# Kernel tuning notes

Hardware: AMD Instinct MI355X
Metric: run time of the kernel (lower is better)

Reference implementation:

```python
import jax, jax.numpy as jnp
import numpy as np

NEG_INF = -jnp.inf


def setup_inputs() -> dict:
    key = jax.random.key(0)
    k1, k2, k3, k4 = jax.random.split(key, 4)
    B, V = 256, 128000
    logits = jax.random.normal(k1, (B, V), dtype=jnp.float32)
    temperatures = jax.random.uniform(k2, (B,), dtype=jnp.float32, minval=0.5, maxval=1.5)
    top_ks = jax.random.randint(k3, (B,), 0, 1024, dtype=jnp.int32)
    top_ps = jax.random.uniform(k4, (B,), dtype=jnp.float32)
    return {"logits": logits, "temperatures": temperatures, "top_ks": top_ks, "top_ps": top_ps}


def _filtered_logits(logits, temperatures, top_ks, top_ps):
    # Faithful vectorized version of the per-row torch loops.
    B, V = logits.shape
    x = logits.astype(jnp.float32) / temperatures[:, None]

    # Sort each row descending once; reuse for top-k and top-p.
    order = jnp.argsort(-x, axis=-1)                       # [B, V] desc indices
    sorted_x = jnp.take_along_axis(x, order, axis=-1)      # [B, V]
    ranks = jnp.arange(V)[None, :]                         # [1, V]

    # top-k: active only when 0 < k < V (matches torch branch)
    k = top_ks[:, None].astype(jnp.int32)
    topk_active = (k > 0) & (k < V)
    keep_k = jnp.where(topk_active, ranks < k, True)
    sorted_x = jnp.where(keep_k, sorted_x, NEG_INF)

    # top-p on softmax of top-k-filtered logits. Softmax is order-preserving,
    # so sorted probs == softmax of sorted (filtered) logits.
    sorted_probs = jax.nn.softmax(sorted_x, axis=-1)
    cumsum = jnp.cumsum(sorted_probs, axis=-1)
    p = top_ps[:, None]
    cutoff = jnp.sum(cumsum <= p, axis=-1, keepdims=True)  # (cumsum<=p).sum()
    cutoff = jnp.where(cutoff < V, cutoff + 1, cutoff)     # include next token
    topp_active = (p > 0.0) & (p < 1.0)
    keep_p = jnp.where(topp_active, ranks < cutoff, True)
    sorted_x = jnp.where(keep_p, sorted_x, NEG_INF)

    # Unsort back to original token order.
    inv = jnp.argsort(order, axis=-1)
    return jnp.take_along_axis(sorted_x, inv, axis=-1)


def reference(logits, temperatures, top_ks, top_ps):
    x = _filtered_logits(logits, temperatures, top_ks, top_ps)
    probs = jax.nn.softmax(x, axis=-1)
    # Gumbel-max style sampling: argmax(probs / Exp(1)) (torch .exponential_ trick)
    e = jax.random.exponential(jax.random.key(42), probs.shape, dtype=jnp.float32)
    e = jnp.maximum(e, 1e-10)
    return jnp.argmax(probs / e, axis=-1)
```

## Files before the change

### kernel.cpp

```cpp
#include <hip/hip_runtime.h>
#include <stdint.h>

#define VV 128000
#define BLOCK 1024
#define NB 4096
#define CAP 4096

typedef unsigned long long ull;

__device__ __forceinline__ uint32_t rotl32(uint32_t x, int r){ return (x << r) | (x >> (32 - r)); }

__device__ __forceinline__ float exp_noise(uint32_t f){
  const uint32_t ks0 = 0u, ks1 = 42u, ks2 = 0x1BD11BDAu ^ 0u ^ 42u;
  uint32_t x0 = 0u + ks0;
  uint32_t x1 = f + ks1;
#define R1(r) { x0 += x1; x1 = rotl32(x1, r); x1 ^= x0; }
  R1(13) R1(15) R1(26) R1(6)   x0 += ks1; x1 += ks2 + 1u;
  R1(17) R1(29) R1(16) R1(24)  x0 += ks2; x1 += ks0 + 2u;
  R1(13) R1(15) R1(26) R1(6)   x0 += ks0; x1 += ks1 + 3u;
  R1(17) R1(29) R1(16) R1(24)  x0 += ks1; x1 += ks2 + 4u;
  R1(13) R1(15) R1(26) R1(6)   x0 += ks2; x1 += ks0 + 5u;
#undef R1
  uint32_t bits = x0 ^ x1;
  float u = __uint_as_float((bits >> 9) | 0x3F800000u) - 1.0f;
  float e = -log1pf(-u);
  return fmaxf(e, 1e-10f);
}

__device__ __forceinline__ uint32_t fkey(float x){
  uint32_t u = __float_as_uint(x);
  return u ^ ((u & 0x80000000u) ? 0xFFFFFFFFu : 0x80000000u);
}
__device__ __forceinline__ float keyval(uint32_t k){
  uint32_t bits = (k & 0x80000000u) ? (k ^ 0x80000000u) : ~k;
  return __uint_as_float(bits);
}

__device__ void suffix_scan_u(uint32_t* h, uint32_t* tmp, int tid){
  const int base = tid * 4;
  uint32_t l0=h[base], l1=h[base+1], l2=h[base+2], l3=h[base+3];
  uint32_t s3=l3, s2=l2+s3, s1=l1+s2, s0=l0+s1;
  tmp[tid] = s0; __syncthreads();
  for (int d=1; d<BLOCK; d<<=1){
    uint32_t add = (tid+d<BLOCK) ? tmp[tid+d] : 0u;
    __syncthreads();
    tmp[tid] += add;
    __syncthreads();
  }
  uint32_t E = (tid+1<BLOCK) ? tmp[tid+1] : 0u;
  h[base]=s0+E; h[base+1]=s1+E; h[base+2]=s2+E; h[base+3]=s3+E;
  __syncthreads();
}
__device__ void suffix_scan_f(float* h, float* tmp, int tid){
  const int base = tid * 4;
  float l0=h[base], l1=h[base+1], l2=h[base+2], l3=h[base+3];
  float s3=l3, s2=l2+s3, s1=l1+s2, s0=l0+s1;
  tmp[tid] = s0; __syncthreads();
  for (int d=1; d<BLOCK; d<<=1){
    float add = (tid+d<BLOCK) ? tmp[tid+d] : 0.f;
    __syncthreads();
    tmp[tid] += add;
    __syncthreads();
  }
  float E = (tid+1<BLOCK) ? tmp[tid+1] : 0.f;
  h[base]=s0+E; h[base+1]=s1+E; h[base+2]=s2+E; h[base+3]=s3+E;
  __syncthreads();
}

__device__ uint32_t select_tth_smallest(uint32_t* a, int n, int t){
  for (int i=0;i<t;i++){
    int mi=i; uint32_t mv=a[i];
    for (int j=i+1;j<n;j++) if (a[j]<mv){ mv=a[j]; mi=j; }
    a[mi]=a[i]; a[i]=mv;
  }
  return a[t-1];
}

__device__ void bitonic_sort(ull* a, int N, int tid){
  for (int len=2; len<=N; len<<=1){
    for (int j=len>>1; j>0; j>>=1){
      for (int i=tid; i<N; i+=BLOCK){
        int l = i ^ j;
        if (l > i){
          ull x = a[i], y = a[l];
          bool asc = ((i & len) == 0);
          if (asc ? (x > y) : (x < y)){ a[i]=y; a[l]=x; }
        }
      }
      __syncthreads();
    }
  }
}

#define ROW4R_BEGIN \
    for (int c0 = tid; c0 < VV/4; c0 += BLOCK*4){ \
      float4 qv[4]; int cb[4]; bool gv[4]; \
      _Pragma("unroll") \
      for (int t=0;t<4;t++){ int cc = c0 + t*BLOCK; gv[t] = (cc < VV/4); cb[t] = cc*4; if (gv[t]) qv[t] = rp[cc]; } \
      _Pragma("unroll") \
      for (int t=0;t<4;t++) if (gv[t]){ \
        float vs[4] = {qv[t].x, qv[t].y, qv[t].z, qv[t].w}; \
        _Pragma("unroll") \
        for (int j=0;j<4;j++){ \
          uint32_t u = fkey(vs[j]); \
          uint32_t idx = (uint32_t)(cb[t]+j); \
          (void)idx;
#define ROW4R_END } } }

#define ROW4_BEGIN \
    for (int c0 = tid; c0 < VV/4; c0 += BLOCK*4){ \
      float4 qv[4]; int cb[4]; bool gv[4]; \
      _Pragma("unroll") \
      for (int t=0;t<4;t++){ int cc = c0 + t*BLOCK; gv[t] = (cc < VV/4); cb[t] = cc*4; if (gv[t]) qv[t] = rp[cc]; } \
      _Pragma("unroll") \
      for (int t=0;t<4;t++) if (gv[t]){ \
        float xs[4] = {qv[t].x, qv[t].y, qv[t].z, qv[t].w}; \
        _Pragma("unroll") \
        for (int j=0;j<4;j++){ \
          float x = xs[j]/T; \
          uint32_t u = fkey(x); \
          uint32_t idx = (uint32_t)(cb[t]+j); \
          (void)idx;
#define ROW4_END } } }

__global__ __launch_bounds__(BLOCK) void sampler_kernel(
    const float* __restrict__ logits, const float* __restrict__ temps,
    const int* __restrict__ topks, const float* __restrict__ topps,
    int* __restrict__ out)
{
  __shared__ __align__(16) uint8_t SM[102400];
  uint32_t* h4    = (uint32_t*)SM;
  ull*      cand  = (ull*)SM;
  uint32_t* h2    = (uint32_t*)(SM + 32*1024);
  ull*      sort2 = (ull*)(SM + 48*1024);
  float*    S     = (float*)SM;
  float*    wf    = (float*)(SM + 16*1024);
  uint32_t* wu    = (uint32_t*)(SM + 64*1024);
  float*    tmpf  = (float*)(SM + 80*1024);
  uint32_t* tmpu  = (uint32_t*)(SM + 84*1024);
  float*    ck    = (float*)(SM + 88*1024);
  ull*      red   = (ull*)(SM + 92*1024);

  __shared__ int s_idx, s_n, s_n2, s_tk, s_ntk, s_tp, s_ntp;
  __shared__ uint32_t s_uk, s_idxk, s_up, s_idxp;
  __shared__ float s_m, s_Zk, s_Ztot;

  const int b   = blockIdx.x;
  const int tid = threadIdx.x;
  const float T = temps[b];
  const int   k = topks[b];
  const float p = topps[b];
  const float* row = logits + (size_t)b * VV;
  const float4* rp = reinterpret_cast<const float4*>(row);
  const bool topk_act = (k > 0) && (k < VV);
  const bool topp_act = (p > 0.0f) && (p < 1.0f);

  if (topk_act){
    for (int i=tid;i<4*NB;i+=BLOCK) h4[i]=0u;
    __syncthreads();
    ROW4R_BEGIN
      atomicAdd(&h4[((u>>20)<<2) | (uint32_t)(tid&3)], 1u);
    ROW4R_END
    __syncthreads();
    for (int i=tid;i<NB;i+=BLOCK)
      wu[i] = h4[(i<<2)] + h4[(i<<2)|1] + h4[(i<<2)|2] + h4[(i<<2)|3];
    __syncthreads();
    suffix_scan_u(wu, tmpu, tid);
    if (tid==0) s_idx = 0;
    __syncthreads();
    for (int i=tid;i<NB;i+=BLOCK){
      uint32_t a  = wu[i];
      uint32_t nn = (i+1<NB) ? wu[i+1] : 0u;
      if (a >= (uint32_t)k && nn < (uint32_t)k) s_idx = i;
    }
    __syncthreads();
    const uint32_t beta = (uint32_t)s_idx;
    const int n = (int)wu[beta];
    const uint32_t c_above = (beta+1<NB) ? wu[beta+1] : 0u;
    if (n <= CAP){
      if (tid==0) s_n = 0;
      __syncthreads();
      ROW4R_BEGIN
        if ((u>>20) >= beta){
          int pos = atomicAdd(&s_n, 1);
          cand[pos] = (((ull)(~u))<<32) | idx;
        }
      ROW4R_END
      __syncthreads();
      ull* srt; int m;
      if (n <= 1024){ srt = cand; m = n; }
      else {
        for (int i=tid;i<NB;i+=BLOCK) h2[i]=0u;
        __syncthreads();
        for (int i=tid;i<n;i+=BLOCK){
          uint32_t u2 = ~(uint32_t)(cand[i]>>32);
          if ((u2>>20) == beta) atomicAdd(&h2[(u2>>8)&0xFFFu], 1u);
        }
        __syncthreads();
        suffix_scan_u(h2, tmpu, tid);
        const uint32_t kr = (uint32_t)k - c_above;
        if (tid==0) s_idx = 0;
        __syncthreads();
        for (int i=tid;i<NB;i+=BLOCK){
          uint32_t a  = h2[i];
          uint32_t nn = (i+1<NB) ? h2[i+1] : 0u;
          if (a >= kr && nn < kr) s_idx = i;
        }
        __syncthreads();
        const uint32_t gam = (uint32_t)s_idx;
        const int np = (int)(c_above + h2[gam]);
        if (np <= 1024){
          if (tid==0) s_n2 = 0;
          __syncthreads();
          const uint32_t cut24 = (beta<<12) | gam;
          for (int i=tid;i<n;i+=BLOCK){
            ull e = cand[i];
            uint32_t u2 = ~(uint32_t)(e>>32);
            if ((u2>>8) >= cut24){
              int pos = atomicAdd(&s_n2, 1);
              sort2[pos] = e;
            }
          }
          __syncthreads();
          srt = sort2; m = np;
        } else { srt = cand; m = n; }
      }
      int N = 2; while (N < m) N <<= 1;
      for (int i=tid;i<N;i+=BLOCK) if (i >= m) srt[i] = 0xFFFFFFFFFFFFFFFFull;
      __syncthreads();
      bitonic_sort(srt, N, tid);
      const int kk = k;
      const float xm = keyval(~(uint32_t)(srt[0]>>32)) / T;
      float w = 0.f; uint32_t myidx = 0u;
      if (tid < kk){
        ull e = srt[tid];
        myidx = (uint32_t)e;
        float xv = keyval(~(uint32_t)(e>>32)) / T;
        w = expf(xv - xm);
      }
      ck[tid] = w; __syncthreads();
      for (int d=BLOCK/2; d>0; d>>=1){
        if (tid < d) ck[tid] += ck[tid+d];
        __syncthreads();
      }
      if (tid==0) s_Ztot = ck[0];
      __syncthreads();
      const float Zk = s_Ztot;
      ck[tid] = w / Zk; __syncthreads();
      for (int d=1; d<BLOCK; d<<=1){
        float add = (tid >= d) ? ck[tid-d] : 0.f;
        __syncthreads();
        ck[tid] += add;
        __syncthreads();
      }
      tmpu[tid] = (tid < kk && ck[tid] <= p) ? 1u : 0u;
      __syncthreads();
      for (int d=BLOCK/2; d>0; d>>=1){
        if (tid < d) tmpu[tid] += tmpu[tid+d];
        __syncthreads();
      }
      int L;
      if (!topp_act) L = kk;
      else { int c = (int)tmpu[0]; L = (c >= kk) ? kk : (c + 1); }
      ull best = 0ull;
      if (tid < L){
        float q = w / exp_noise((uint32_t)b * (uint32_t)VV + myidx);
        best = (((ull)__float_as_uint(q)) << 32) | (uint32_t)(~myidx);
      }
      red[tid] = best; __syncthreads();
      for (int d=BLOCK/2; d>0; d>>=1){
        if (tid < d){ ull o = red[tid+d]; if (o > red[tid]) red[tid] = o; }
        __syncthreads();
      }
      if (tid==0) out[b] = (int)(~(uint32_t)(red[0] & 0xFFFFFFFFull));
      return;
    }
    __syncthreads();
  }

  for (int i=tid;i<NB;i+=BLOCK){ S[i]=0.f; wu[i]=0u; }
  __syncthreads();
  float lmax = -3.4e38f;
  ROW4_BEGIN
    lmax = fmaxf(lmax, x);
    atomicAdd(&wu[u>>20], 1u);
    atomicAdd(&S[u>>20], expf(x));
  ROW4_END
  tmpf[tid] = lmax; __syncthreads();
  for (int d=BLOCK/2; d>0; d>>=1){
    if (tid < d) tmpf[tid] = fmaxf(tmpf[tid], tmpf[tid+d]);
    __syncthreads();
  }
  if (tid==0) s_m = tmpf[0];
  __syncthreads();
  suffix_scan_u(wu, tmpu, tid);
  suffix_scan_f(S,  tmpf, tid);

  uint32_t uk = 0u, idxk = 0xFFFFFFFFu;
  int bk1 = -1;
  if (topk_act){
    if (tid==0) s_idx = 0;
    __syncthreads();
    for (int i=tid;i<NB;i+=BLOCK){
      uint32_t a  = wu[i];
      uint32_t nn = (i+1<NB) ? wu[i+1] : 0u;
      if (a >= (uint32_t)k && nn < (uint32_t)k) s_idx = i;
    }
    __syncthreads();
    bk1 = s_idx;
    const uint32_t c_above1 = (bk1+1<NB) ? wu[bk1+1] : 0u;
    const float    M_above1 = (bk1+1<NB) ? S[bk1+1]  : 0.f;
    __syncthreads();
    for (int i=tid;i<NB;i+=BLOCK){ wu[i]=0u; wf[i]=0.f; }
    __syncthreads();
    ROW4_BEGIN
      if ((int)(u>>20) == bk1){
        atomicAdd(&wu[(u>>8)&0xFFFu], 1u);
        atomicAdd(&wf[(u>>8)&0xFFFu], expf(x));
      }
    ROW4_END
    __syncthreads();
    suffix_scan_u(wu, tmpu, tid);
    suffix_scan_f(wf, tmpf, tid);
    if (tid==0) s_idx = 0;
    __syncthreads();
    for (int i=tid;i<NB;i+=BLOCK){
      uint32_t a  = c_above1 + wu[i];
      uint32_t nn = c_above1 + ((i+1<NB) ? wu[i+1] : 0u);
      if (a >= (uint32_t)k && nn < (uint32_t)k) s_idx = i;
    }
    __syncthreads();
    const int bk2 = s_idx;
    const uint32_t c_above2 = c_above1 + ((bk2+1<NB) ? wu[bk2+1] : 0u);
    const float    M_above2 = M_above1 + ((bk2+1<NB) ? wf[bk2+1] : 0.f);
    __syncthreads();
    if (tid < 256){ wu[tid]=0u; wf[tid]=0.f; }
    __syncthreads();
    const uint32_t top24k = (((uint32_t)bk1)<<12) | (uint32_t)bk2;
    ROW4_BEGIN
      if ((u>>8) == top24k){
        atomicAdd(&wu[u & 0xFFu], 1u);
        atomicAdd(&wf[u & 0xFFu], expf(x));
      }
    ROW4_END
    __syncthreads();
    if (tid==0){
      uint32_t r = 0u; float mr = 0.f; int b3 = 0;
      for (int i=255;i>=0;--i){
        if (c_above2 + r + wu[i] >= (uint32_t)k){ b3 = i; break; }
        r += wu[i]; mr += wf[i];
      }
      const uint32_t cgt = c_above2 + r;
      const float mgt = M_above2 + mr;
      const int nt = (int)wu[b3];
      const int tk = k - (int)cgt;
      s_uk  = (((uint32_t)bk1)<<20) | (((uint32_t)bk2)<<8) | (uint32_t)b3;
      s_tk  = tk; s_ntk = nt;
      s_Zk  = mgt + (float)tk * expf(keyval(s_uk));
      s_n   = 0;
    }
    __syncthreads();
    uk = s_uk;
    if (s_tk < s_ntk){
      ROW4_BEGIN
        if (u == uk){
          int pos = atomicAdd(&s_n, 1);
          if (pos < NB) wu[pos] = idx;
        }
      ROW4_END
      __syncthreads();
      if (tid==0){
        int n2 = min(s_n, NB);
        int t  = min(s_tk, n2);
        s_idxk = select_tth_smallest(wu, n2, t);
      }
      __syncthreads();
      idxk = s_idxk;
    }
  }
  const float Zk = topk_act ? s_Zk : S[0];

  uint32_t up = 0u, idxp = 0xFFFFFFFFu;
  const float tgt = p * Zk;
  const bool pall = (!topp_act) || (tgt >= Zk);
  if (!pall){
    if (tid==0) s_idx = -2;
    __syncthreads();
    for (int i=tid;i<NB;i+=BLOCK){
      if (i > bk1){
        float a  = S[i];
        float nn = (i+1<NB) ? S[i+1] : 0.f;
        if (a > tgt && nn <= tgt) s_idx = i;
      }
    }
    __syncthreads();
    int bp1 = (s_idx >= 0) ? s_idx : bk1;
    if (bp1 < 0) bp1 = 0;
    const float Mab = (bp1+1<NB) ? S[bp1+1] : 0.f;
    __syncthreads();
    for (int i=tid;i<NB;i+=BLOCK) wf[i]=0.f;
    __syncthreads();
    ROW4_BEGIN
      if ((int)(u>>20) == bp1){
        bool kk_ok = (!topk_act) || (u > uk) || (u == uk && idx <= idxk);
        if (kk_ok) atomicAdd(&wf[(u>>8)&0xFFFu], expf(x));
      }
    ROW4_END
    __syncthreads();
    suffix_scan_f(wf, tmpf, tid);
    if (tid==0) s_idx = -2;
    __syncthreads();
    for (int i=tid;i<NB;i+=BLOCK){
      float a  = Mab + wf[i];
      float nn = Mab + ((i+1<NB) ? wf[i+1] : 0.f);
      if (a > tgt && nn <= tgt) s_idx = i;
    }
    __syncthreads();
    int bp2;
    if (s_idx >= 0){ bp2 = s_idx; }
    else {
      if (tid==0) s_idx = NB;
      __syncthreads();
      for (int i=tid;i<NB;i+=BLOCK){
        float a  = wf[i];
        float nn = (i+1<NB) ? wf[i+1] : 0.f;
        if (a > nn) atomicMin(&s_idx, i);
      }
      __syncthreads();
      bp2 = (s_idx < NB) ? s_idx : 0;
    }
    const float Mab2 = Mab + ((bp2+1<NB) ? wf[bp2+1] : 0.f);
    __syncthreads();
    if (tid < 256){ wf[tid]=0.f; wu[tid]=0u; }
    __syncthreads();
    const uint32_t top24p = (((uint32_t)bp1)<<12) | (uint32_t)bp2;
    ROW4_BEGIN
      if ((u>>8) == top24p){
        bool kk_ok = (!topk_act) || (u > uk) || (u == uk && idx <= idxk);
        if (kk_ok){
          atomicAdd(&wf[u & 0xFFu], expf(x));
          atomicAdd(&wu[u & 0xFFu], 1u);
        }
      }
    ROW4_END
    __syncthreads();
    if (tid==0){
      float run = 0.f; int b3 = -1; float mgt = 0.f;
      for (int i=255;i>=0;--i){
        float sufn = run; run += wf[i];
        if (Mab2 + run > tgt && Mab2 + sufn <= tgt){ b3 = i; mgt = Mab2 + sufn; break; }
      }
      if (b3 < 0){
        float run2 = 0.f;
        for (int i=255;i>=0;--i){
          if (wu[i] > 0u){ b3 = i; mgt = Mab2 + run2; }
          run2 += wf[i];
        }
        if (b3 < 0){ b3 = 0; mgt = Mab2; }
      }
      const uint32_t upv = (((uint32_t)bp1)<<20) | (((uint32_t)bp2)<<8) | (uint32_t)b3;
      const int ntp = (int)wu[b3];
      const float ev = expf(keyval(upv));
      int t = 0;
      for (int j=1;j<=ntp;j++){
        float before = mgt + (float)(j-1) * ev;
        if (before / Zk <= p) t++; else break;
      }
      if (t < 1) t = 1;
      s_up = upv; s_tp = t; s_ntp = ntp; s_n = 0;
    }
    __syncthreads();
    up = s_up;
    if (s_tp < s_ntp){
      ROW4_BEGIN
        if (u == up){
          bool kk_ok = (!topk_act) || (u > uk) || (u == uk && idx <= idxk);
          if (kk_ok){
            int pos = atomicAdd(&s_n, 1);
            if (pos < NB) wu[pos] = idx;
          }
        }
      ROW4_END
      __syncthreads();
      if (tid==0){
        int n2 = min(s_n, NB);
        int t  = min(s_tp, n2);
        s_idxp = select_tth_smallest(wu, n2, t);
      }
      __syncthreads();
      idxp = s_idxp;
    }
  }

  const float m  = s_m;
  const float Zs = Zk * expf(-m);
  ull best = 0ull;
  ROW4_BEGIN
    bool kk_ok = (!topk_act) || (u > uk) || (u == uk && idx <= idxk);
    bool kp_ok = pall || (u > up) || (u == up && idx <= idxp);
    if (kk_ok && kp_ok){
      float q = (expf(x - m) / Zs) / exp_noise((uint32_t)b * (uint32_t)VV + idx);
      ull pk = (((ull)__float_as_uint(q)) << 32) | (uint32_t)(~idx);
      best = (pk > best) ? pk : best;
    }
  ROW4_END
  red[tid] = best; __syncthreads();
  for (int d=BLOCK/2; d>0; d>>=1){
    if (tid < d){ ull o = red[tid+d]; if (o > red[tid]) red[tid] = o; }
    __syncthreads();
  }
  if (tid==0) out[b] = (int)(~(uint32_t)(red[0] & 0xFFFFFFFFull));
}

extern "C" void kernel_launch(void* const* d_in, const int* in_sizes, int n_in,
                              void* d_out, int out_size, void* d_ws, size_t ws_size,
                              hipStream_t stream) {
  (void)in_sizes; (void)n_in; (void)out_size; (void)d_ws; (void)ws_size;
  const float* logits = (const float*)d_in[0];
  const float* temps  = (const float*)d_in[1];
  const int*   ks     = (const int*)d_in[2];
  const float* ps     = (const float*)d_in[3];
  int* out = (int*)d_out;
  sampler_kernel<<<256, BLOCK, 0, stream>>>(logits, temps, ks, ps, out);
}
```

Before: 231.5 us.

## Split sampler into multi-kernel pipeline with per-row chunked histogram and candidate gather

```diff
diff --git a/kernel.cpp b/kernel.cpp
--- a/kernel.cpp
+++ b/kernel.cpp
@@ -2,9 +2,10 @@
 #include <stdint.h>
 
 #define VV 128000
-#define BLOCK 1024
-#define NB 4096
+#define HN 4096
 #define CAP 4096
+#define CAPR 8192
+#define CHUNK_F4 4000
 
 typedef unsigned long long ull;
 
@@ -36,18 +37,375 @@
   return __uint_as_float(bits);
 }
 
+__device__ uint32_t select_tth_smallest(uint32_t* a, int n, int t){
+  for (int i=0;i<t;i++){
+    int mi=i; uint32_t mv=a[i];
+    for (int j=i+1;j<n;j++) if (a[j]<mv){ mv=a[j]; mi=j; }
+    a[mi]=a[i]; a[i]=mv;
+  }
+  return a[t-1];
+}
+
+template<typename Tv, int NT>
+__device__ __forceinline__ void suffix4096(Tv* h, Tv* parts, int tid){
+  constexpr int E = HN/NT;
+  const int base = tid*E;
+  Tv loc[E]; Tv s = (Tv)0;
+  #pragma unroll
+  for (int i=E-1;i>=0;--i){ s += h[base+i]; loc[i]=s; }
+  const int lane = tid & 63, w = tid >> 6;
+  Tv v = s;
+  #pragma unroll
+  for (int d=1; d<64; d<<=1){
+    Tv o = __shfl_down(v, (unsigned)d, 64);
+    if (lane + d < 64) v += o;
+  }
+  if (lane == 0) parts[w] = v;
+  __syncthreads();
+  Tv woff = (Tv)0;
+  for (int i=w+1;i<NT/64;i++) woff += parts[i];
+  Tv lex = __shfl_down(v, 1u, 64);
+  if (lane == 63) lex = (Tv)0;
+  const Tv off = woff + lex;
+  #pragma unroll
+  for (int i=0;i<E;i++) h[base+i] = loc[i] + off;
+  __syncthreads();
+}
+
+__global__ __launch_bounds__(256) void hist_kernel(const float* __restrict__ logits,
+                                                   uint32_t* __restrict__ hists){
+  __shared__ uint32_t h[HN];
+  const int g = blockIdx.x, r = g >> 3, c = g & 7, tid = threadIdx.x;
+  for (int i=tid;i<HN;i+=256) h[i]=0u;
+  __syncthreads();
+  const float4* rp = reinterpret_cast<const float4*>(logits + (size_t)r*VV) + (size_t)c*CHUNK_F4;
+  for (int c0=tid;c0<CHUNK_F4;c0+=1024){
+    float4 q[4]; bool g4[4];
+    #pragma unroll
+    for (int t=0;t<4;t++){ int cc=c0+t*256; g4[t]=(cc<CHUNK_F4); if(g4[t]) q[t]=rp[cc]; }
+    #pragma unroll
+    for (int t=0;t<4;t++) if(g4[t]){
+      atomicAdd(&h[fkey(q[t].x)>>20],1u);
+      atomicAdd(&h[fkey(q[t].y)>>20],1u);
+      atomicAdd(&h[fkey(q[t].z)>>20],1u);
+      atomicAdd(&h[fkey(q[t].w)>>20],1u);
+    }
+  }
+  __syncthreads();
+  uint32_t* gh = hists + (size_t)r*HN;
+  for (int i=tid;i<HN;i+=256){ uint32_t v=h[i]; if (v) atomicAdd(&gh[i], v); }
+}
+
+__global__ __launch_bounds__(256) void gather_kernel(const float* __restrict__ logits,
+    const int* __restrict__ topks, const uint32_t* __restrict__ hists,
+    uint32_t* __restrict__ ctrs, ull* __restrict__ cands){
+  __shared__ uint32_t h[HN];
+  __shared__ uint32_t parts[4];
+  __shared__ int s_beta;
+  const int g = blockIdx.x, r = g >> 3, c = g & 7, tid = threadIdx.x;
+  const int k = topks[r];
+  if (k < 1 || k >= VV) return;
+  const uint32_t* gh = hists + (size_t)r*HN;
+  for (int i=tid;i<HN;i+=256) h[i] = gh[i];
+  __syncthreads();
+  suffix4096<uint32_t,256>(h, parts, tid);
+  if (tid==0) s_beta = 0;
+  __syncthreads();
+  for (int i=tid;i<HN;i+=256){
+    uint32_t a=h[i], nn=(i+1<HN)?h[i+1]:0u;
+    if (a >= (uint32_t)k && nn < (uint32_t)k) s_beta=i;
+  }
+  __syncthreads();
+  const uint32_t beta=(uint32_t)s_beta;
+  const uint32_t n = h[beta];
+  if (n > CAPR){ if (c==0 && tid==0) ctrs[r] = n; return; }
+  ull* cr = cands + (size_t)r*CAPR;
+  const float4* rp = reinterpret_cast<const float4*>(logits + (size_t)r*VV) + (size_t)c*CHUNK_F4;
+  const uint32_t idx0 = (uint32_t)(c*CHUNK_F4*4);
+  for (int c0=tid;c0<CHUNK_F4;c0+=1024){
+    float4 q[4]; bool g4[4];
+    #pragma unroll
+    for (int t=0;t<4;t++){ int cc=c0+t*256; g4[t]=(cc<CHUNK_F4); if(g4[t]) q[t]=rp[cc]; }
+    #pragma unroll
+    for (int t=0;t<4;t++) if(g4[t]){
+      float vs[4]={q[t].x,q[t].y,q[t].z,q[t].w};
+      #pragma unroll
+      for (int j=0;j<4;j++){
+        uint32_t u=fkey(vs[j]);
+        if ((u>>20) >= beta){
+          uint32_t pos = atomicAdd(&ctrs[r], 1u);
+          cr[pos] = (((ull)u)<<32) | (idx0 + (uint32_t)(c0+t*256)*4u + (uint32_t)j);
+        }
+      }
+    }
+  }
+}
+
+__global__ __launch_bounds__(1024) void select_kernel(
+    const float* __restrict__ temps, const int* __restrict__ topks, const float* __restrict__ topps,
+    const uint32_t* __restrict__ ctrs, const ull* __restrict__ cands, int* __restrict__ outp){
+  __shared__ ull ce[CAPR];
+  __shared__ uint32_t hbu[HN];
+  __shared__ uint32_t c3[256];
+  __shared__ float    f3[256];
+  __shared__ uint32_t tie[2048];
+  __shared__ uint32_t parts_u[16];
+  __shared__ float    parts_f[16];
+  __shared__ ull      parts_m[16];
+  __shared__ int s_i1, s_i2, s_nt, s_tp, s_ntp, s_cnt;
+  __shared__ uint32_t s_um, s_uk, s_idxk, s_up, s_idxp, s_cgt;
+  __shared__ float s_Zk;
+
+  const int r = blockIdx.x, tid = threadIdx.x;
+  const int k = topks[r];
+  if (k < 1 || k >= VV) return;
+  const uint32_t ntot = ctrs[r];
+  if (ntot > CAPR) return;
+  const int n = (int)ntot;
+  const float T = temps[r];
+  const float p = topps[r];
+  const bool topp_act = (p > 0.f) && (p < 1.f);
+  const ull* cr = cands + (size_t)r*CAPR;
+  for (int i=tid;i<n;i+=1024) ce[i] = cr[i];
+  __syncthreads();
+
+  uint32_t um = 0u;
+  for (int i=tid;i<n;i+=1024){ uint32_t u=(uint32_t)(ce[i]>>32); um = um>u?um:u; }
+  {
+    const int lane=tid&63, w=tid>>6; uint32_t v=um;
+    #pragma unroll
+    for (int d=32;d>0;d>>=1){ uint32_t o=__shfl_down(v,(unsigned)d,64); if(lane+d<64 && o>v) v=o; }
+    if (lane==0) parts_u[w]=v;
+    __syncthreads();
+    if (tid==0){ uint32_t m2=0; for(int i=0;i<16;i++) if(parts_u[i]>m2) m2=parts_u[i]; s_um=m2; }
+    __syncthreads();
+    um = s_um;
+  }
+  const float xm = keyval(um)/T;
+
+  for (int i=tid;i<HN;i+=1024) hbu[i]=0u;
+  __syncthreads();
+  for (int i=tid;i<n;i+=1024){ uint32_t u=(uint32_t)(ce[i]>>32); atomicAdd(&hbu[u>>20],1u); }
+  __syncthreads();
+  suffix4096<uint32_t,1024>(hbu, parts_u, tid);
+  if (tid==0) s_i1=0;
+  __syncthreads();
+  for (int i=tid;i<HN;i+=1024){
+    uint32_t a=hbu[i], nn=(i+1<HN)?hbu[i+1]:0u;
+    if (a>=(uint32_t)k && nn<(uint32_t)k) s_i1=i;
+  }
+  __syncthreads();
+  const int b1=s_i1;
+  const uint32_t cA=(b1+1<HN)?hbu[b1+1]:0u;
+  __syncthreads();
+  for (int i=tid;i<HN;i+=1024) hbu[i]=0u;
+  __syncthreads();
+  for (int i=tid;i<n;i+=1024){ uint32_t u=(uint32_t)(ce[i]>>32); if ((int)(u>>20)==b1) atomicAdd(&hbu[(u>>8)&0xFFFu],1u); }
+  __syncthreads();
+  suffix4096<uint32_t,1024>(hbu, parts_u, tid);
+  if (tid==0) s_i2=0;
+  __syncthreads();
+  for (int i=tid;i<HN;i+=1024){
+    uint32_t a=cA+hbu[i], nn=cA+((i+1<HN)?hbu[i+1]:0u);
+    if (a>=(uint32_t)k && nn<(uint32_t)k) s_i2=i;
+  }
+  __syncthreads();
+  const int b2=s_i2;
+  const uint32_t cB=cA+((b2+1<HN)?hbu[b2+1]:0u);
+  if (tid<256) c3[tid]=0u;
+  __syncthreads();
+  const uint32_t t24=((uint32_t)b1<<12)|(uint32_t)b2;
+  for (int i=tid;i<n;i+=1024){ uint32_t u=(uint32_t)(ce[i]>>32); if ((u>>8)==t24) atomicAdd(&c3[u&0xFFu],1u); }
+  __syncthreads();
+  if (tid==0){
+    uint32_t rr=0; int b3=0;
+    for (int i=255;i>=0;--i){ if (cB+rr+c3[i] >= (uint32_t)k){ b3=i; break; } rr+=c3[i]; }
+    s_uk=(t24<<8)|(uint32_t)b3;
+    s_cgt=cB+rr;
+    s_nt=(int)c3[b3];
+    s_cnt=0;
+  }
+  __syncthreads();
+  const uint32_t uk=s_uk;
+  const int tk=k-(int)s_cgt, nt=s_nt;
+  uint32_t idxk=0xFFFFFFFFu;
+  if (tk<nt){
+    for (int i=tid;i<n;i+=1024){
+      ull e=ce[i]; uint32_t u=(uint32_t)(e>>32);
+      if (u==uk){ int pos=atomicAdd(&s_cnt,1); if (pos<2048) tie[pos]=(uint32_t)e; }
+    }
+    __syncthreads();
+    if (tid==0){
+      int m2=min(s_cnt,2048); int t=min(tk,m2);
+      s_idxk=select_tth_smallest(tie,m2,t);
+    }
+    __syncthreads();
+    idxk=s_idxk;
+  }
+  float zpart=0.f;
+  for (int i=tid;i<n;i+=1024){
+    ull e=ce[i]; uint32_t u=(uint32_t)(e>>32); uint32_t idx=(uint32_t)e;
+    if ((u>uk)||(u==uk&&idx<=idxk)) zpart += expf(keyval(u)/T - xm);
+  }
+  {
+    const int lane=tid&63,w=tid>>6; float v=zpart;
+    #pragma unroll
+    for (int d=32;d>0;d>>=1){ float o=__shfl_down(v,(unsigned)d,64); if(lane+d<64) v+=o; }
+    if (lane==0) parts_f[w]=v;
+    __syncthreads();
+    if (tid==0){ float z=0.f; for(int i=0;i<16;i++) z+=parts_f[i]; s_Zk=z; }
+    __syncthreads();
+  }
+  const float Zk=s_Zk;
+
+  uint32_t up=0u, idxp=0xFFFFFFFFu;
+  const float tgt=p*Zk;
+  const bool pall=(!topp_act)||(tgt>=Zk);
+  if (!pall){
+    float* hbf=(float*)hbu;
+    for (int i=tid;i<HN;i+=1024) hbf[i]=0.f;
+    __syncthreads();
+    for (int i=tid;i<n;i+=1024){
+      ull e=ce[i]; uint32_t u=(uint32_t)(e>>32); uint32_t idx=(uint32_t)e;
+      if ((u>uk)||(u==uk&&idx<=idxk)) atomicAdd(&hbf[u>>20], expf(keyval(u)/T-xm));
+    }
+    __syncthreads();
+    suffix4096<float,1024>(hbf, parts_f, tid);
+    if (tid==0) s_i1=-1;
+    __syncthreads();
+    for (int i=tid;i<HN;i+=1024){
+      float a=hbf[i], nn=(i+1<HN)?hbf[i+1]:0.f;
+      if (a>tgt && nn<=tgt) s_i1=i;
+    }
+    __syncthreads();
+    int bp1=s_i1;
+    if (bp1<0){
+      if (tid==0) s_i1=HN;
+      __syncthreads();
+      for (int i=tid;i<HN;i+=1024){
+        float a=hbf[i], nn=(i+1<HN)?hbf[i+1]:0.f;
+        if (a>nn) atomicMin(&s_i1,i);
+      }
+      __syncthreads();
+      bp1=(s_i1<HN)?s_i1:0;
+    }
+    const float Mab=(bp1+1<HN)?hbf[bp1+1]:0.f;
+    __syncthreads();
+    for (int i=tid;i<HN;i+=1024) hbf[i]=0.f;
+    __syncthreads();
+    for (int i=tid;i<n;i+=1024){
+      ull e=ce[i]; uint32_t u=(uint32_t)(e>>32); uint32_t idx=(uint32_t)e;
+      if ((int)(u>>20)==bp1 && ((u>uk)||(u==uk&&idx<=idxk)))
+        atomicAdd(&hbf[(u>>8)&0xFFFu], expf(keyval(u)/T-xm));
+    }
+    __syncthreads();
+    suffix4096<float,1024>(hbf, parts_f, tid);
+    if (tid==0) s_i2=-1;
+    __syncthreads();
+    for (int i=tid;i<HN;i+=1024){
+      float a=Mab+hbf[i], nn=Mab+((i+1<HN)?hbf[i+1]:0.f);
+      if (a>tgt && nn<=tgt) s_i2=i;
+    }
+    __syncthreads();
+    int bp2=s_i2;
+    if (bp2<0){
+      if (tid==0) s_i2=HN;
+      __syncthreads();
+      for (int i=tid;i<HN;i+=1024){
+        float a=hbf[i], nn=(i+1<HN)?hbf[i+1]:0.f;
+        if (a>nn) atomicMin(&s_i2,i);
+      }
+      __syncthreads();
+      bp2=(s_i2<HN)?s_i2:0;
+    }
+    const float Mab2=Mab+((bp2+1<HN)?hbf[bp2+1]:0.f);
+    __syncthreads();
+    if (tid<256){ f3[tid]=0.f; c3[tid]=0u; }
+    __syncthreads();
+    const uint32_t p24=((uint32_t)bp1<<12)|(uint32_t)bp2;
+    for (int i=tid;i<n;i+=1024){
+      ull e=ce[i]; uint32_t u=(uint32_t)(e>>32); uint32_t idx=(uint32_t)e;
+      if ((u>>8)==p24 && ((u>uk)||(u==uk&&idx<=idxk))){
+        atomicAdd(&f3[u&0xFFu], expf(keyval(u)/T-xm));
+        atomicAdd(&c3[u&0xFFu],1u);
+      }
+    }
+    __syncthreads();
+    if (tid==0){
+      float run=0.f; int b3=-1; float mgt=0.f;
+      for (int i=255;i>=0;--i){
+        float sufn=run; run+=f3[i];
+        if (Mab2+run>tgt && Mab2+sufn<=tgt){ b3=i; mgt=Mab2+sufn; break; }
+      }
+      if (b3<0){
+        float run2=0.f;
+        for (int i=255;i>=0;--i){ if (c3[i]>0u){ b3=i; mgt=Mab2+run2; } run2+=f3[i]; }
+        if (b3<0){ b3=0; mgt=Mab2; }
+      }
+      const uint32_t upv=(p24<<8)|(uint32_t)b3;
+      const int ntp=(int)c3[b3];
+      const float ev=expf(keyval(upv)/T - xm);
+      int t=0;
+      for (int j=1;j<=ntp;j++){ float before=mgt+(float)(j-1)*ev; if (before<=tgt) t++; else break; }
+      if (t<1) t=1;
+      s_up=upv; s_tp=t; s_ntp=ntp; s_cnt=0;
+    }
+    __syncthreads();
+    up=s_up;
+    if (s_tp<s_ntp){
+      for (int i=tid;i<n;i+=1024){
+        ull e=ce[i]; uint32_t u=(uint32_t)(e>>32); uint32_t idx=(uint32_t)e;
+        if (u==up && ((u>uk)||(u==uk&&idx<=idxk))){
+          int pos=atomicAdd(&s_cnt,1); if (pos<2048) tie[pos]=idx;
+        }
+      }
+      __syncthreads();
+      if (tid==0){
+        int m2=min(s_cnt,2048); int t=min(s_tp,m2);
+        s_idxp=select_tth_smallest(tie,m2,t);
+      }
+      __syncthreads();
+      idxp=s_idxp;
+    }
+  }
+
+  ull best=0ull;
+  for (int i=tid;i<n;i+=1024){
+    ull e=ce[i]; uint32_t u=(uint32_t)(e>>32); uint32_t idx=(uint32_t)e;
+    bool kk=(u>uk)||(u==uk&&idx<=idxk);
+    bool kp=pall||(u>up)||(u==up&&idx<=idxp);
+    if (kk&&kp){
+      float w=expf(keyval(u)/T-xm);
+      float q=w/exp_noise((uint32_t)r*(uint32_t)VV+idx);
+      ull pk=(((ull)__float_as_uint(q))<<32)|(uint32_t)(~idx);
+      best=(pk>best)?pk:best;
+    }
+  }
+  {
+    const int lane=tid&63,w=tid>>6; ull v=best;
+    #pragma unroll
+    for (int d=32;d>0;d>>=1){ ull o=__shfl_down(v,(unsigned)d,64); if(lane+d<64 && o>v) v=o; }
+    if (lane==0) parts_m[w]=v;
+    __syncthreads();
+    if (tid==0){
+      ull m2=0ull; for(int i=0;i<16;i++) if (parts_m[i]>m2) m2=parts_m[i];
+      outp[r]=(int)(~(uint32_t)(m2 & 0xFFFFFFFFull));
+    }
+  }
+}
+
 __device__ void suffix_scan_u(uint32_t* h, uint32_t* tmp, int tid){
   const int base = tid * 4;
   uint32_t l0=h[base], l1=h[base+1], l2=h[base+2], l3=h[base+3];
   uint32_t s3=l3, s2=l2+s3, s1=l1+s2, s0=l0+s1;
   tmp[tid] = s0; __syncthreads();
-  for (int d=1; d<BLOCK; d<<=1){
-    uint32_t add = (tid+d<BLOCK) ? tmp[tid+d] : 0u;
+  for (int d=1; d<1024; d<<=1){
+    uint32_t add = (tid+d<1024) ? tmp[tid+d] : 0u;
     __syncthreads();
     tmp[tid] += add;
     __syncthreads();
   }
-  uint32_t E = (tid+1<BLOCK) ? tmp[tid+1] : 0u;
+  uint32_t E = (tid+1<1024) ? tmp[tid+1] : 0u;
   h[base]=s0+E; h[base+1]=s1+E; h[base+2]=s2+E; h[base+3]=s3+E;
   __syncthreads();
 }
@@ -56,30 +414,21 @@
   float l0=h[base], l1=h[base+1], l2=h[base+2], l3=h[base+3];
   float s3=l3, s2=l2+s3, s1=l1+s2, s0=l0+s1;
   tmp[tid] = s0; __syncthreads();
-  for (int d=1; d<BLOCK; d<<=1){
-    float add = (tid+d<BLOCK) ? tmp[tid+d] : 0.f;
+  for (int d=1; d<1024; d<<=1){
+    float add = (tid+d<1024) ? tmp[tid+d] : 0.f;
     __syncthreads();
     tmp[tid] += add;
     __syncthreads();
   }
-  float E = (tid+1<BLOCK) ? tmp[tid+1] : 0.f;
+  float E = (tid+1<1024) ? tmp[tid+1] : 0.f;
   h[base]=s0+E; h[base+1]=s1+E; h[base+2]=s2+E; h[base+3]=s3+E;
   __syncthreads();
-}
-
-__device__ uint32_t select_tth_smallest(uint32_t* a, int n, int t){
-  for (int i=0;i<t;i++){
-    int mi=i; uint32_t mv=a[i];
-    for (int j=i+1;j<n;j++) if (a[j]<mv){ mv=a[j]; mi=j; }
-    a[mi]=a[i]; a[i]=mv;
-  }
-  return a[t-1];
 }
 
 __device__ void bitonic_sort(ull* a, int N, int tid){
   for (int len=2; len<=N; len<<=1){
     for (int j=len>>1; j>0; j>>=1){
-      for (int i=tid; i<N; i+=BLOCK){
+      for (int i=tid; i<N; i+=1024){
         int l = i ^ j;
         if (l > i){
           ull x = a[i], y = a[l];
@@ -93,10 +442,10 @@
 }
 
 #define ROW4R_BEGIN \
-    for (int c0 = tid; c0 < VV/4; c0 += BLOCK*4){ \
+    for (int c0 = tid; c0 < VV/4; c0 += 1024*4){ \
       float4 qv[4]; int cb[4]; bool gv[4]; \
       _Pragma("unroll") \
-      for (int t=0;t<4;t++){ int cc = c0 + t*BLOCK; gv[t] = (cc < VV/4); cb[t] = cc*4; if (gv[t]) qv[t] = rp[cc]; } \
+      for (int t=0;t<4;t++){ int cc = c0 + t*1024; gv[t] = (cc < VV/4); cb[t] = cc*4; if (gv[t]) qv[t] = rp[cc]; } \
       _Pragma("unroll") \
       for (int t=0;t<4;t++) if (gv[t]){ \
         float vs[4] = {qv[t].x, qv[t].y, qv[t].z, qv[t].w}; \
@@ -108,10 +457,10 @@
 #define ROW4R_END } } }
 
 #define ROW4_BEGIN \
-    for (int c0 = tid; c0 < VV/4; c0 += BLOCK*4){ \
+    for (int c0 = tid; c0 < VV/4; c0 += 1024*4){ \
       float4 qv[4]; int cb[4]; bool gv[4]; \
       _Pragma("unroll") \
-      for (int t=0;t<4;t++){ int cc = c0 + t*BLOCK; gv[t] = (cc < VV/4); cb[t] = cc*4; if (gv[t]) qv[t] = rp[cc]; } \
+      for (int t=0;t<4;t++){ int cc = c0 + t*1024; gv[t] = (cc < VV/4); cb[t] = cc*4; if (gv[t]) qv[t] = rp[cc]; } \
       _Pragma("unroll") \
       for (int t=0;t<4;t++) if (gv[t]){ \
         float xs[4] = {qv[t].x, qv[t].y, qv[t].z, qv[t].w}; \
@@ -123,10 +472,10 @@
           (void)idx;
 #define ROW4_END } } }
 
-__global__ __launch_bounds__(BLOCK) void sampler_kernel(
+__global__ __launch_bounds__(1024) void sampler_kernel(
     const float* __restrict__ logits, const float* __restrict__ temps,
     const int* __restrict__ topks, const float* __restrict__ topps,
-    int* __restrict__ out)
+    int* __restrict__ out, const uint32_t* __restrict__ ctrs, int mode)
 {
   __shared__ __align__(16) uint8_t SM[102400];
   uint32_t* h4    = (uint32_t*)SM;
@@ -155,28 +504,31 @@
   const bool topk_act = (k > 0) && (k < VV);
   const bool topp_act = (p > 0.0f) && (p < 1.0f);
 
-  if (topk_act){
-    for (int i=tid;i<4*NB;i+=BLOCK) h4[i]=0u;
+  const bool ovf = (mode==1) && topk_act && (ctrs[b] > CAPR);
+  if (mode==1 && topk_act && !ovf) return;
+
+  if (mode==0 && topk_act){
+    for (int i=tid;i<4*HN;i+=1024) h4[i]=0u;
     __syncthreads();
     ROW4R_BEGIN
       atomicAdd(&h4[((u>>20)<<2) | (uint32_t)(tid&3)], 1u);
     ROW4R_END
     __syncthreads();
-    for (int i=tid;i<NB;i+=BLOCK)
+    for (int i=tid;i<HN;i+=1024)
       wu[i] = h4[(i<<2)] + h4[(i<<2)|1] + h4[(i<<2)|2] + h4[(i<<2)|3];
     __syncthreads();
     suffix_scan_u(wu, tmpu, tid);
     if (tid==0) s_idx = 0;
     __syncthreads();
-    for (int i=tid;i<NB;i+=BLOCK){
+    for (int i=tid;i<HN;i+=1024){
       uint32_t a  = wu[i];
-      uint32_t nn = (i+1<NB) ? wu[i+1] : 0u;
+      uint32_t nn = (i+1<HN) ? wu[i+1] : 0u;
       if (a >= (uint32_t)k && nn < (uint32_t)k) s_idx = i;
     }
     __syncthreads();
     const uint32_t beta = (uint32_t)s_idx;
     const int n = (int)wu[beta];
-    const uint32_t c_above = (beta+1<NB) ? wu[beta+1] : 0u;
+    const uint32_t c_above = (beta+1<HN) ? wu[beta+1] : 0u;
     if (n <= CAP){
       if (tid==0) s_n = 0;
       __syncthreads();
@@ -190,9 +542,9 @@
       ull* srt; int m;
       if (n <= 1024){ srt = cand; m = n; }
       else {
-        for (int i=tid;i<NB;i+=BLOCK) h2[i]=0u;
+        for (int i=tid;i<HN;i+=1024) h2[i]=0u;
         __syncthreads();
-        for (int i=tid;i<n;i+=BLOCK){
+        for (int i=tid;i<n;i+=1024){
           uint32_t u2 = ~(uint32_t)(cand[i]>>32);
           if ((u2>>20) == beta) atomicAdd(&h2[(u2>>8)&0xFFFu], 1u);
         }
@@ -201,9 +553,9 @@
         const uint32_t kr = (uint32_t)k - c_above;
         if (tid==0) s_idx = 0;
         __syncthreads();
-        for (int i=tid;i<NB;i+=BLOCK){
+        for (int i=tid;i<HN;i+=1024){
           uint32_t a  = h2[i];
-          uint32_t nn = (i+1<NB) ? h2[i+1] : 0u;
+          uint32_t nn = (i+1<HN) ? h2[i+1] : 0u;
           if (a >= kr && nn < kr) s_idx = i;
         }
         __syncthreads();
@@ -213,7 +565,7 @@
           if (tid==0) s_n2 = 0;
           __syncthreads();
           const uint32_t cut24 = (beta<<12) | gam;
-          for (int i=tid;i<n;i+=BLOCK){
+          for (int i=tid;i<n;i+=1024){
             ull e = cand[i];
             uint32_t u2 = ~(uint32_t)(e>>32);
             if ((u2>>8) >= cut24){
@@ -226,7 +578,7 @@
         } else { srt = cand; m = n; }
       }
       int N = 2; while (N < m) N <<= 1;
-      for (int i=tid;i<N;i+=BLOCK) if (i >= m) srt[i] = 0xFFFFFFFFFFFFFFFFull;
+      for (int i=tid;i<N;i+=1024) if (i >= m) srt[i] = 0xFFFFFFFFFFFFFFFFull;
       __syncthreads();
       bitonic_sort(srt, N, tid);
       const int kk = k;
@@ -239,7 +591,7 @@
         w = expf(xv - xm);
       }
       ck[tid] = w; __syncthreads();
-      for (int d=BLOCK/2; d>0; d>>=1){
+      for (int d=512; d>0; d>>=1){
         if (tid < d) ck[tid] += ck[tid+d];
         __syncthreads();
       }
@@ -247,7 +599,7 @@
       __syncthreads();
       const float Zk = s_Ztot;
       ck[tid] = w / Zk; __syncthreads();
-      for (int d=1; d<BLOCK; d<<=1){
+      for (int d=1; d<1024; d<<=1){
         float add = (tid >= d) ? ck[tid-d] : 0.f;
         __syncthreads();
         ck[tid] += add;
@@ -255,7 +607,7 @@
       }
       tmpu[tid] = (tid < kk && ck[tid] <= p) ? 1u : 0u;
       __syncthreads();
-      for (int d=BLOCK/2; d>0; d>>=1){
+      for (int d=512; d>0; d>>=1){
         if (tid < d) tmpu[tid] += tmpu[tid+d];
         __syncthreads();
       }
@@ -268,7 +620,7 @@
         best = (((ull)__float_as_uint(q)) << 32) | (uint32_t)(~myidx);
       }
       red[tid] = best; __syncthreads();
-      for (int d=BLOCK/2; d>0; d>>=1){
+      for (int d=512; d>0; d>>=1){
         if (tid < d){ ull o = red[tid+d]; if (o > red[tid]) red[tid] = o; }
         __syncthreads();
       }
@@ -278,7 +630,7 @@
     __syncthreads();
   }
 
-  for (int i=tid;i<NB;i+=BLOCK){ S[i]=0.f; wu[i]=0u; }
+  for (int i=tid;i<HN;i+=1024){ S[i]=0.f; wu[i]=0u; }
   __syncthreads();
   float lmax = -3.4e38f;
   ROW4_BEGIN
@@ -287,7 +639,7 @@
     atomicAdd(&S[u>>20], expf(x));
   ROW4_END
   tmpf[tid] = lmax; __syncthreads();
-  for (int d=BLOCK/2; d>0; d>>=1){
+  for (int d=512; d>0; d>>=1){
     if (tid < d) tmpf[tid] = fmaxf(tmpf[tid], tmpf[tid+d]);
     __syncthreads();
   }
@@ -301,17 +653,17 @@
   if (topk_act){
     if (tid==0) s_idx = 0;
     __syncthreads();
-    for (int i=tid;i<NB;i+=BLOCK){
+    for (int i=tid;i<HN;i+=1024){
       uint32_t a  = wu[i];
-      uint32_t nn = (i+1<NB) ? wu[i+1] : 0u;
+      uint32_t nn = (i+1<HN) ? wu[i+1] : 0u;
       if (a >= (uint32_t)k && nn < (uint32_t)k) s_idx = i;
     }
     __syncthreads();
     bk1 = s_idx;
-    const uint32_t c_above1 = (bk1+1<NB) ? wu[bk1+1] : 0u;
-    const float    M_above1 = (bk1+1<NB) ? S[bk1+1]  : 0.f;
-    __syncthreads();
-    for (int i=tid;i<NB;i+=BLOCK){ wu[i]=0u; wf[i]=0.f; }
+    const uint32_t c_above1 = (bk1+1<HN) ? wu[bk1+1] : 0u;
+    const float    M_above1 = (bk1+1<HN) ? S[bk1+1]  : 0.f;
+    __syncthreads();
+    for (int i=tid;i<HN;i+=1024){ wu[i]=0u; wf[i]=0.f; }
     __syncthreads();
     ROW4_BEGIN
       if ((int)(u>>20) == bk1){
@@ -324,15 +676,15 @@
     suffix_scan_f(wf, tmpf, tid);
     if (tid==0) s_idx = 0;
     __syncthreads();
-    for (int i=tid;i<NB;i+=BLOCK){
+    for (int i=tid;i<HN;i+=1024){
       uint32_t a  = c_above1 + wu[i];
-      uint32_t nn = c_above1 + ((i+1<NB) ? wu[i+1] : 0u);
+      uint32_t nn = c_above1 + ((i+1<HN) ? wu[i+1] : 0u);
       if (a >= (uint32_t)k && nn < (uint32_t)k) s_idx = i;
     }
     __syncthreads();
     const int bk2 = s_idx;
-    const uint32_t c_above2 = c_above1 + ((bk2+1<NB) ? wu[bk2+1] : 0u);
-    const float    M_above2 = M_above1 + ((bk2+1<NB) ? wf[bk2+1] : 0.f);
+    const uint32_t c_above2 = c_above1 + ((bk2+1<HN) ? wu[bk2+1] : 0u);
+    const float    M_above2 = M_above1 + ((bk2+1<HN) ? wf[bk2+1] : 0.f);
     __syncthreads();
     if (tid < 256){ wu[tid]=0u; wf[tid]=0.f; }
     __syncthreads();
@@ -365,12 +717,12 @@
       ROW4_BEGIN
         if (u == uk){
           int pos = atomicAdd(&s_n, 1);
-          if (pos < NB) wu[pos] = idx;
+          if (pos < HN) wu[pos] = idx;
         }
       ROW4_END
       __syncthreads();
       if (tid==0){
-        int n2 = min(s_n, NB);
+        int n2 = min(s_n, HN);
         int t  = min(s_tk, n2);
         s_idxk = select_tth_smallest(wu, n2, t);
       }
@@ -386,19 +738,19 @@
   if (!pall){
     if (tid==0) s_idx = -2;
     __syncthreads();
-    for (int i=tid;i<NB;i+=BLOCK){
+    for (int i=tid;i<HN;i+=1024){
       if (i > bk1){
         float a  = S[i];
-        float nn = (i+1<NB) ? S[i+1] : 0.f;
+        float nn = (i+1<HN) ? S[i+1] : 0.f;
         if (a > tgt && nn <= tgt) s_idx = i;
       }
     }
     __syncthreads();
     int bp1 = (s_idx >= 0) ? s_idx : bk1;
     if (bp1 < 0) bp1 = 0;
-    const float Mab = (bp1+1<NB) ? S[bp1+1] : 0.f;
-    __syncthreads();
-    for (int i=tid;i<NB;i+=BLOCK) wf[i]=0.f;
+    const float Mab = (bp1+1<HN) ? S[bp1+1] : 0.f;
+    __syncthreads();
+    for (int i=tid;i<HN;i+=1024) wf[i]=0.f;
     __syncthreads();
     ROW4_BEGIN
       if ((int)(u>>20) == bp1){
@@ -410,26 +762,26 @@
     suffix_scan_f(wf, tmpf, tid);
     if (tid==0) s_idx = -2;
     __syncthreads();
-    for (int i=tid;i<NB;i+=BLOCK){
+    for (int i=tid;i<HN;i+=1024){
       float a  = Mab + wf[i];
-      float nn = Mab + ((i+1<NB) ? wf[i+1] : 0.f);
+      float nn = Mab + ((i+1<HN) ? wf[i+1] : 0.f);
       if (a > tgt && nn <= tgt) s_idx = i;
     }
     __syncthreads();
     int bp2;
     if (s_idx >= 0){ bp2 = s_idx; }
     else {
-      if (tid==0) s_idx = NB;
-      __syncthreads();
-      for (int i=tid;i<NB;i+=BLOCK){
+      if (tid==0) s_idx = HN;
+      __syncthreads();
+      for (int i=tid;i<HN;i+=1024){
         float a  = wf[i];
-        float nn = (i+1<NB) ? wf[i+1] : 0.f;
+        float nn = (i+1<HN) ? wf[i+1] : 0.f;
         if (a > nn) atomicMin(&s_idx, i);
       }
       __syncthreads();
-      bp2 = (s_idx < NB) ? s_idx : 0;
-    }
-    const float Mab2 = Mab + ((bp2+1<NB) ? wf[bp2+1] : 0.f);
+      bp2 = (s_idx < HN) ? s_idx : 0;
+    }
+    const float Mab2 = Mab + ((bp2+1<HN) ? wf[bp2+1] : 0.f);
     __syncthreads();
     if (tid < 256){ wf[tid]=0.f; wu[tid]=0u; }
     __syncthreads();
@@ -477,13 +829,13 @@
           bool kk_ok = (!topk_act) || (u > uk) || (u == uk && idx <= idxk);
           if (kk_ok){
             int pos = atomicAdd(&s_n, 1);
-            if (pos < NB) wu[pos] = idx;
+            if (pos < HN) wu[pos] = idx;
           }
         }
       ROW4_END
       __syncthreads();
       if (tid==0){
-        int n2 = min(s_n, NB);
+        int n2 = min(s_n, HN);
         int t  = min(s_tp, n2);
         s_idxp = select_tth_smallest(wu, n2, t);
       }
@@ -505,7 +857,7 @@
     }
   ROW4_END
   red[tid] = best; __syncthreads();
-  for (int d=BLOCK/2; d>0; d>>=1){
+  for (int d=512; d>0; d>>=1){
     if (tid < d){ ull o = red[tid+d]; if (o > red[tid]) red[tid] = o; }
     __syncthreads();
   }
@@ -515,11 +867,29 @@
 extern "C" void kernel_launch(void* const* d_in, const int* in_sizes, int n_in,
                               void* d_out, int out_size, void* d_ws, size_t ws_size,
                               hipStream_t stream) {
-  (void)in_sizes; (void)n_in; (void)out_size; (void)d_ws; (void)ws_size;
+  (void)in_sizes; (void)n_in; (void)out_size;
   const float* logits = (const float*)d_in[0];
   const float* temps  = (const float*)d_in[1];
   const int*   ks     = (const int*)d_in[2];
   const float* ps     = (const float*)d_in[3];
   int* out = (int*)d_out;
-  sampler_kernel<<<256, BLOCK, 0, stream>>>(logits, temps, ks, ps, out);
-}
+
+  const size_t HIST_BYTES = (size_t)256*HN*4;
+  const size_t CTR_BYTES  = 1024;
+  const size_t CAND_BYTES = (size_t)256*CAPR*8;
+  const size_t NEED = HIST_BYTES + CTR_BYTES + CAND_BYTES;
+
+  if (ws_size >= NEED && d_ws != nullptr){
+    uint8_t* ws = (uint8_t*)d_ws;
+    uint32_t* hists = (uint32_t*)ws;
+    uint32_t* ctrs  = (uint32_t*)(ws + HIST_BYTES);
+    ull*      cands = (ull*)(ws + HIST_BYTES + CTR_BYTES);
+    hipMemsetAsync(ws, 0, HIST_BYTES + CTR_BYTES, stream);
+    hist_kernel  <<<2048, 256, 0, stream>>>(logits, hists);
+    gather_kernel<<<2048, 256, 0, stream>>>(logits, ks, hists, ctrs, cands);
+    select_kernel<<<256, 1024, 0, stream>>>(temps, ks, ps, ctrs, cands, out);
+    sampler_kernel<<<256, 1024, 0, stream>>>(logits, temps, ks, ps, out, ctrs, 1);
+  } else {
+    sampler_kernel<<<256, 1024, 0, stream>>>(logits, temps, ks, ps, out, nullptr, 0);
+  }
+}
```

Result: slower. 478.5 us (+106.7%).
